# Kernel optimization log

Hardware: AMD Instinct MI355X
Metric: run time of the kernel (lower is better)

The kernel has to match this reference:

```python
import jax, jax.numpy as jnp
import numpy as np

EMBED = 1024
HEADS = 16
HEAD_DIM = EMBED // HEADS


def setup_inputs() -> dict:
    key = jax.random.key(0)
    ks = jax.random.split(key, 9)
    s = 1.0 / np.sqrt(EMBED)
    x = jax.random.normal(ks[0], (2, 2048, EMBED), dtype=jnp.float32)
    Wq = jax.random.uniform(ks[1], (EMBED, EMBED), jnp.float32, -s, s)
    bq = jax.random.uniform(ks[2], (EMBED,), jnp.float32, -s, s)
    Wk = jax.random.uniform(ks[3], (EMBED, EMBED), jnp.float32, -s, s)
    bk = jax.random.uniform(ks[4], (EMBED,), jnp.float32, -s, s)
    Wv = jax.random.uniform(ks[5], (EMBED, EMBED), jnp.float32, -s, s)
    bv = jax.random.uniform(ks[6], (EMBED,), jnp.float32, -s, s)
    Wo = jax.random.uniform(ks[7], (EMBED, EMBED), jnp.float32, -s, s)
    bo = jax.random.uniform(ks[8], (EMBED,), jnp.float32, -s, s)
    return {"x": x, "Wq": Wq, "bq": bq, "Wk": Wk, "bk": bk,
            "Wv": Wv, "bv": bv, "Wo": Wo, "bo": bo}


def reference(x, Wq, bq, Wk, bk, Wv, bv, Wo, bo):
    B, S, E = x.shape
    H, D = HEADS, HEAD_DIM
    # QKV projections, split heads: [B,S,E] -> [B,H,S,D]
    def proj(W, b):
        return (x @ W + b).reshape(B, S, H, D).transpose(0, 2, 1, 3)
    q, k, v = proj(Wq, bq), proj(Wk, bk), proj(Wv, bv)
    scores = jnp.einsum('bhsd,bhtd->bhst', q, k) / jnp.sqrt(jnp.float32(D))
    attn = jax.nn.softmax(scores, axis=-1)
    out = jnp.einsum('bhst,bhtd->bhsd', attn, v)  # [B,H,S,D]
    out = out.transpose(0, 2, 1, 3).reshape(B, S, E)
    return out @ Wo + bo
```

## Files before the change

kernel.cpp:

```cpp
#include <hip/hip_runtime.h>
#include <cstddef>
#include <cstdint>

#define EMB 1024
#define NH 16
#define HD 64
#define SEQ 2048
#define BATCH 2
#define MROWS 4096
#define LOG2E 1.4426950408889634f

typedef unsigned short u16;
typedef __attribute__((ext_vector_type(8))) short short8;
typedef __attribute__((ext_vector_type(4))) short short4v;
typedef __attribute__((ext_vector_type(4))) float floatx4;

#define MFMA32(a,b,c) __builtin_amdgcn_mfma_f32_16x16x32_bf16((a),(b),(c),0,0,0)

#if __has_builtin(__builtin_amdgcn_mfma_f32_16x16x16bf16_1k)
#define PVMFMA(a,b,c) __builtin_amdgcn_mfma_f32_16x16x16bf16_1k((a),(b),(c),0,0,0)
#elif __has_builtin(__builtin_amdgcn_mfma_f32_16x16x16_bf16)
#define PVMFMA(a,b,c) __builtin_amdgcn_mfma_f32_16x16x16_bf16((a),(b),(c),0,0,0)
#else
__device__ __forceinline__ floatx4 pv_mfma_fb(short4v a, short4v b, floatx4 c) {
    short8 a8 = {a.x, a.y, a.z, a.w, 0, 0, 0, 0};
    short8 b8 = {b.x, b.y, b.z, b.w, 0, 0, 0, 0};
    return MFMA32(a8, b8, c);
}
#define PVMFMA(a,b,c) pv_mfma_fb((a),(b),(c))
#endif

__device__ __forceinline__ u16 f2bf(float f) {
    union { float f; uint32_t u; } v; v.f = f;
    return (u16)((v.u + 0x7fffu + ((v.u >> 16) & 1u)) >> 16);
}
__device__ __forceinline__ uint32_t pk_trunc(float a, float b) {
    union { float f; uint32_t u; } va, vb; va.f = a; vb.f = b;
    return __builtin_amdgcn_perm(vb.u, va.u, 0x07060302u);
}
__device__ __forceinline__ float lo_f(uint32_t u) {
    union { uint32_t u; float f; } v; v.u = u << 16; return v.f;
}
__device__ __forceinline__ float hi_f(uint32_t u) {
    union { uint32_t u; float f; } v; v.u = u & 0xffff0000u; return v.f;
}
typedef const __attribute__((address_space(1))) void* gptr_t;
typedef __attribute__((address_space(3))) void* lptr_t;
__device__ __forceinline__ void gl2lds16(const void* g, void* l) {
    __builtin_amdgcn_global_load_lds((gptr_t)g, (lptr_t)l, 16, 0, 0);
}

__global__ __launch_bounds__(256) void cvt_all_k(
    const float* __restrict__ x,
    const float* __restrict__ W0, const float* __restrict__ W1,
    const float* __restrict__ W2, const float* __restrict__ W3,
    u16* __restrict__ Wt4, u16* __restrict__ xh) {
    const int z = blockIdx.z;
    const int tid = threadIdx.x;
    if (z == 4) {
        const int nb = gridDim.x * gridDim.y;
        const int bid = blockIdx.y * gridDim.x + blockIdx.x;
        const int stride = nb * 256 * 8;
        for (int i = (bid * 256 + tid) * 8; i < MROWS * EMB; i += stride) {
            float4 a = *(const float4*)(x + i);
            float4 b = *(const float4*)(x + i + 4);
            alignas(16) u16 o[8] = {f2bf(a.x), f2bf(a.y), f2bf(a.z), f2bf(a.w),
                                    f2bf(b.x), f2bf(b.y), f2bf(b.z), f2bf(b.w)};
            *(uint4*)(xh + i) = *(const uint4*)o;
        }
        return;
    }
    const float* W = (z == 0) ? W0 : (z == 1) ? W1 : (z == 2) ? W2 : W3;
    const float scale = (z == 0) ? 0.125f * LOG2E : 1.0f;
    u16* dst = Wt4 + (size_t)z * 1048576;
    __shared__ float Lf[64][65];
    const int kt = blockIdx.y * 64, nt = blockIdx.x * 64;
    {
        const int r = tid >> 2, c4 = (tid & 3) * 16;
        const float* src = W + (size_t)(kt + r) * EMB + nt + c4;
        #pragma unroll
        for (int i = 0; i < 16; i += 4) {
            float4 v = *(const float4*)(src + i);
            Lf[r][c4 + i + 0] = v.x; Lf[r][c4 + i + 1] = v.y;
            Lf[r][c4 + i + 2] = v.z; Lf[r][c4 + i + 3] = v.w;
        }
    }
    __syncthreads();
    const int n = tid >> 2, k4 = (tid & 3) * 16;
    alignas(16) u16 hb[16];
    #pragma unroll
    for (int i = 0; i < 16; ++i) hb[i] = f2bf(Lf[k4 + i][n] * scale);
    const size_t o = (size_t)(nt + n) * EMB + kt + k4;
    *(uint4*)(dst + o) = *(const uint4*)hb;
    *(uint4*)(dst + o + 8) = *(const uint4*)(hb + 8);
}

__global__ __launch_bounds__(256) void gemm_qkv_k(
    const u16* __restrict__ xh, const u16* __restrict__ Wt4,
    const float* __restrict__ b0, const float* __restrict__ b1,
    const float* __restrict__ b2,
    u16* __restrict__ Q, u16* __restrict__ K, u16* __restrict__ Vt) {
    const int z = blockIdx.z;
    const u16* Wt = Wt4 + (size_t)z * 1048576;
    const float* bias = (z == 0) ? b0 : (z == 1) ? b1 : b2;
    const float bscale = (z == 0) ? 0.125f * LOG2E : 1.0f;
    const int bm = blockIdx.y * 128, bn = blockIdx.x * 128;
    __shared__ alignas(16) u16 As[4096];
    __shared__ alignas(16) u16 Bs[4096];
    const int tid = threadIdx.x;
    const int lane = tid & 63, w = tid >> 6;
    const int l15 = lane & 15, quad = lane >> 4;
    const int wm = (w & 1) * 64, wn = (w >> 1) * 64;

    floatx4 acc[4][4];
    const floatx4 zf = {0.f, 0.f, 0.f, 0.f};
    #pragma unroll
    for (int mt = 0; mt < 4; ++mt)
        #pragma unroll
        for (int nt = 0; nt < 4; ++nt) acc[mt][nt] = zf;

    const int c0 = tid, c1 = tid + 256;
    const int r0 = c0 >> 2, p0 = c0 & 3, cc0 = (p0 - r0 - (r0 >> 2)) & 3;
    const int r1 = c1 >> 2, p1 = c1 & 3, cc1 = (p1 - r1 - (r1 >> 2)) & 3;
    const u16* ag0 = xh + (size_t)(bm + r0) * EMB + cc0 * 8;
    const u16* ag1 = xh + (size_t)(bm + r1) * EMB + cc1 * 8;
    const u16* bg0 = Wt + (size_t)(bn + r0) * EMB + cc0 * 8;
    const u16* bg1 = Wt + (size_t)(bn + r1) * EMB + cc1 * 8;

    for (int kt = 0; kt < EMB; kt += 32) {
        __syncthreads();
        gl2lds16(ag0 + kt, &As[c0 * 8]); gl2lds16(ag1 + kt, &As[c1 * 8]);
        gl2lds16(bg0 + kt, &Bs[c0 * 8]); gl2lds16(bg1 + kt, &Bs[c1 * 8]);
        __syncthreads();
        short8 af[4], bf[4];
        #pragma unroll
        for (int t = 0; t < 4; ++t) {
            const int ra = wm + t * 16 + l15;
            const int rb = wn + t * 16 + l15;
            af[t] = *(const short8*)&As[ra * 32 + ((quad + ra + (ra >> 2)) & 3) * 8];
            bf[t] = *(const short8*)&Bs[rb * 32 + ((quad + rb + (rb >> 2)) & 3) * 8];
        }
        #pragma unroll
        for (int mt = 0; mt < 4; ++mt)
            #pragma unroll
            for (int nt = 0; nt < 4; ++nt)
                acc[mt][nt] = MFMA32(af[mt], bf[nt], acc[mt][nt]);
    }

    if (z != 2) {
        u16* out = (z == 0) ? Q : K;
        #pragma unroll
        for (int nt = 0; nt < 4; ++nt) {
            const int col = bn + wn + nt * 16 + l15;
            const float bv = bias[col] * bscale;
            #pragma unroll
            for (int mt = 0; mt < 4; ++mt) {
                const int row = bm + wm + mt * 16 + quad * 4;
                #pragma unroll
                for (int r = 0; r < 4; ++r)
                    out[(size_t)(row + r) * EMB + col] = f2bf(acc[mt][nt][r] + bv);
            }
        }
    } else {
        #pragma unroll
        for (int nt = 0; nt < 4; ++nt) {
            const int col = bn + wn + nt * 16 + l15;
            const int hh = col >> 6, d = col & 63;
            const float bv = bias[col];
            #pragma unroll
            for (int mt = 0; mt < 4; ++mt) {
                const int row = bm + wm + mt * 16 + quad * 4;
                const int bb = row >> 11, t0 = row & 2047;
                alignas(8) u16 pk4[4];
                #pragma unroll
                for (int r = 0; r < 4; ++r) pk4[r] = f2bf(acc[mt][nt][r] + bv);
                *(uint2*)(Vt + ((size_t)((bb * NH + hh) * HD + d)) * SEQ + t0) =
                    *(const uint2*)pk4;
            }
        }
    }
}

__global__ __launch_bounds__(256) void gemm_o_k(
    const u16* __restrict__ Ag, const u16* __restrict__ Wt,
    const float* __restrict__ bias, float* __restrict__ out) {
    const int bm = blockIdx.y * 128, bn = blockIdx.x * 64;
    __shared__ alignas(16) u16 As[4096];
    __shared__ alignas(16) u16 Bs[2048];
    const int tid = threadIdx.x;
    const int lane = tid & 63, w = tid >> 6;
    const int l15 = lane & 15, quad = lane >> 4;
    const int wm = w * 32;

    floatx4 acc[2][4];
    const floatx4 zf = {0.f, 0.f, 0.f, 0.f};
    #pragma unroll
    for (int mt = 0; mt < 2; ++mt)
        #pragma unroll
        for (int nt = 0; nt < 4; ++nt) acc[mt][nt] = zf;

    const int c0 = tid, c1 = tid + 256;
    const int r0 = c0 >> 2, p0 = c0 & 3, cc0 = (p0 - r0 - (r0 >> 2)) & 3;
    const int r1 = c1 >> 2, p1 = c1 & 3, cc1 = (p1 - r1 - (r1 >> 2)) & 3;
    const u16* ag0 = Ag + (size_t)(bm + r0) * EMB + cc0 * 8;
    const u16* ag1 = Ag + (size_t)(bm + r1) * EMB + cc1 * 8;
    const u16* bg0 = Wt + (size_t)(bn + r0) * EMB + cc0 * 8;

    for (int kt = 0; kt < EMB; kt += 32) {
        __syncthreads();
        gl2lds16(ag0 + kt, &As[c0 * 8]);
        gl2lds16(ag1 + kt, &As[c1 * 8]);
        if (c0 < 256) gl2lds16(bg0 + kt, &Bs[c0 * 8]);
        __syncthreads();
        short8 af[2], bf[4];
        #pragma unroll
        for (int t = 0; t < 2; ++t) {
            const int ra = wm + t * 16 + l15;
            af[t] = *(const short8*)&As[ra * 32 + ((quad + ra + (ra >> 2)) & 3) * 8];
        }
        #pragma unroll
        for (int t = 0; t < 4; ++t) {
            const int rb = t * 16 + l15;
            bf[t] = *(const short8*)&Bs[rb * 32 + ((quad + rb + (rb >> 2)) & 3) * 8];
        }
        #pragma unroll
        for (int mt = 0; mt < 2; ++mt)
            #pragma unroll
            for (int nt = 0; nt < 4; ++nt)
                acc[mt][nt] = MFMA32(af[mt], bf[nt], acc[mt][nt]);
    }

    #pragma unroll
    for (int nt = 0; nt < 4; ++nt) {
        const int col = bn + nt * 16 + l15;
        const float bv = bias[col];
        #pragma unroll
        for (int mt = 0; mt < 2; ++mt) {
            const int row = bm + wm + mt * 16 + quad * 4;
            #pragma unroll
            for (int r = 0; r < 4; ++r)
                out[(size_t)(row + r) * EMB + col] = acc[mt][nt][r] + bv;
        }
    }
}

__global__ __launch_bounds__(256) void flash_k(
    const u16* __restrict__ Q, const u16* __restrict__ K,
    const u16* __restrict__ Vt,
    u16* __restrict__ Np0, u16* __restrict__ Np1,
    u16* __restrict__ Np2, u16* __restrict__ Np3,
    float* __restrict__ Lp) {
    const int qt = blockIdx.x, h = blockIdx.y;
    const int b = blockIdx.z >> 2, sp = blockIdx.z & 3;
    const int t0 = sp * (SEQ / 4);
    __shared__ alignas(16) u16 Ks[4096];
    __shared__ alignas(16) u16 Vs[4096];
    const int tid = threadIdx.x;
    const int lane = tid & 63, w = tid >> 6;
    const int l15 = lane & 15, quad = lane >> 4;

    const u16* qp = Q + (size_t)(b * SEQ + qt * 128 + w * 32 + l15) * EMB + h * HD + quad * 8;
    short8 qb[2][2];
    qb[0][0] = *(const short8*)qp;
    qb[0][1] = *(const short8*)(qp + 32);
    qb[1][0] = *(const short8*)(qp + 16 * EMB);
    qb[1][1] = *(const short8*)(qp + 16 * EMB + 32);

    const floatx4 zf = {0.f, 0.f, 0.f, 0.f};
    floatx4 oacc[2][4];
    float l_part[2] = {0.f, 0.f};
    #pragma unroll
    for (int u = 0; u < 2; ++u)
        #pragma unroll
        for (int nt = 0; nt < 4; ++nt) oacc[u][nt] = zf;

    const int s0 = tid, s1 = tid + 256;
    const int kr0 = s0 >> 3, kc0 = ((s0 & 7) - kr0) & 7;
    const int kr1 = s1 >> 3, kc1 = ((s1 & 7) - kr1) & 7;
    const u16* kg0 = K + (size_t)(b * SEQ + t0 + kr0) * EMB + h * HD + kc0 * 8;
    const u16* kg1 = K + (size_t)(b * SEQ + t0 + kr1) * EMB + h * HD + kc1 * 8;
    const u16* vg0 = Vt + ((size_t)((b * NH + h) * HD + kr0)) * SEQ + t0 + kc0 * 8;
    const u16* vg1 = Vt + ((size_t)((b * NH + h) * HD + kr1)) * SEQ + t0 + kc1 * 8;

    for (int kt = 0; kt < SEQ / 4 / 64; ++kt) {
        __syncthreads();
        gl2lds16(kg0 + (size_t)kt * 64 * EMB, &Ks[s0 * 8]);
        gl2lds16(kg1 + (size_t)kt * 64 * EMB, &Ks[s1 * 8]);
        gl2lds16(vg0 + kt * 64, &Vs[s0 * 8]);
        gl2lds16(vg1 + kt * 64, &Vs[s1 * 8]);
        __syncthreads();

        floatx4 sa[2][4];
        #pragma unroll
        for (int mt = 0; mt < 4; ++mt) {
            const int r = mt * 16 + l15;
            const short8 ka0 = *(const short8*)&Ks[r * 64 + ((quad + r) & 7) * 8];
            const short8 ka1 = *(const short8*)&Ks[r * 64 + ((quad + 4 + r) & 7) * 8];
            #pragma unroll
            for (int u = 0; u < 2; ++u)
                sa[u][mt] = MFMA32(ka1, qb[u][1], MFMA32(ka0, qb[u][0], zf));
        }

        short4v pfr[2][4];
        #pragma unroll
        for (int u = 0; u < 2; ++u)
            #pragma unroll
            for (int mt = 0; mt < 4; ++mt) {
                const float e0 = exp2f(sa[u][mt][0]);
                const float e1 = exp2f(sa[u][mt][1]);
                const float e2 = exp2f(sa[u][mt][2]);
                const float e3 = exp2f(sa[u][mt][3]);
                const uint32_t u01 = pk_trunc(e0, e1);
                const uint32_t u23 = pk_trunc(e2, e3);
                l_part[u] += (lo_f(u01) + hi_f(u01)) + (lo_f(u23) + hi_f(u23));
                union { uint32_t uu[2]; short4v s; } pk;
                pk.uu[0] = u01; pk.uu[1] = u23;
                pfr[u][mt] = pk.s;
            }

        #pragma unroll
        for (int mt = 0; mt < 4; ++mt) {
            const int c16 = mt * 2 + (quad >> 1);
            const int hof = (quad & 1) * 4;
            #pragma unroll
            for (int nt = 0; nt < 4; ++nt) {
                const int vr = nt * 16 + l15;
                const short4v vb =
                    *(const short4v*)&Vs[vr * 64 + ((c16 + vr) & 7) * 8 + hof];
                #pragma unroll
                for (int u = 0; u < 2; ++u)
                    oacc[u][nt] = PVMFMA(pfr[u][mt], vb, oacc[u][nt]);
            }
        }
    }

    u16* np = (sp == 0) ? Np0 : (sp == 1) ? Np1 : (sp == 2) ? Np2 : Np3;
    float* lp = Lp + (size_t)sp * (MROWS * NH);

    #pragma unroll
    for (int u = 0; u < 2; ++u) {
        l_part[u] += __shfl_xor(l_part[u], 16, 64);
        l_part[u] += __shfl_xor(l_part[u], 32, 64);
        if (quad == 0) {
            const int qrow = qt * 128 + w * 32 + u * 16 + l15;
            lp[(size_t)(b * SEQ + qrow) * NH + h] = l_part[u];
        }
    }

    #pragma unroll
    for (int u = 0; u < 2; ++u)
        #pragma unroll
        for (int r = 0; r < 4; ++r) {
            const size_t o =
                (size_t)(b * SEQ + qt * 128 + w * 32 + u * 16 + quad * 4 + r) * EMB
                + h * HD + l15;
            #pragma unroll
            for (int nt = 0; nt < 4; ++nt)
                np[o + nt * 16] = f2bf(oacc[u][nt][r]);
        }
}

__global__ __launch_bounds__(256) void reduce_k(
    const u16* __restrict__ Np0, const u16* __restrict__ Np1,
    const u16* __restrict__ Np2, const u16* __restrict__ Np3,
    const float* __restrict__ Lp, u16* __restrict__ AO) {
    const int i = blockIdx.x * 256 + threadIdx.x;
    const int e = i * 4;
    const int row = e >> 10;
    const int hh = (e & 1023) >> 6;
    const size_t lx = (size_t)row * NH + hh;
    const float lsum = Lp[lx] + Lp[(size_t)(MROWS * NH) + lx] +
                       Lp[2 * (size_t)(MROWS * NH) + lx] +
                       Lp[3 * (size_t)(MROWS * NH) + lx];
    const float inv = 1.f / lsum;
    const uint2 n0 = *(const uint2*)(Np0 + e);
    const uint2 n1 = *(const uint2*)(Np1 + e);
    const uint2 n2 = *(const uint2*)(Np2 + e);
    const uint2 n3 = *(const uint2*)(Np3 + e);
    const float x0 = (lo_f(n0.x) + lo_f(n1.x) + lo_f(n2.x) + lo_f(n3.x)) * inv;
    const float x1 = (hi_f(n0.x) + hi_f(n1.x) + hi_f(n2.x) + hi_f(n3.x)) * inv;
    const float x2 = (lo_f(n0.y) + lo_f(n1.y) + lo_f(n2.y) + lo_f(n3.y)) * inv;
    const float x3 = (hi_f(n0.y) + hi_f(n1.y) + hi_f(n2.y) + hi_f(n3.y)) * inv;
    uint2 o;
    o.x = (uint32_t)f2bf(x0) | ((uint32_t)f2bf(x1) << 16);
    o.y = (uint32_t)f2bf(x2) | ((uint32_t)f2bf(x3) << 16);
    *(uint2*)(AO + e) = o;
}

extern "C" void kernel_launch(void* const* d_in, const int* in_sizes, int n_in,
                              void* d_out, int out_size, void* d_ws, size_t ws_size,
                              hipStream_t stream) {
    const float* x  = (const float*)d_in[0];
    const float* Wq = (const float*)d_in[1];
    const float* bq = (const float*)d_in[2];
    const float* Wk = (const float*)d_in[3];
    const float* bk = (const float*)d_in[4];
    const float* Wv = (const float*)d_in[5];
    const float* bv = (const float*)d_in[6];
    const float* Wo = (const float*)d_in[7];
    const float* bo = (const float*)d_in[8];

    u16* ws16 = (u16*)d_ws;
    const size_t P4 = (size_t)MROWS * EMB;
    u16* xh  = ws16;
    u16* Qb  = ws16 + P4;
    u16* Kb  = ws16 + 2 * P4;
    u16* Vtb = ws16 + 3 * P4;
    u16* Wt4 = ws16 + 4 * P4;
    u16* N1  = ws16 + 5 * P4;
    u16* N2  = ws16 + 6 * P4;
    u16* N3  = ws16 + 7 * P4;
    float* Lp = (float*)(ws16 + 8 * P4);

    cvt_all_k<<<dim3(16, 16, 5), 256, 0, stream>>>(x, Wq, Wk, Wv, Wo, Wt4, xh);
    gemm_qkv_k<<<dim3(8, 32, 3), 256, 0, stream>>>(xh, Wt4, bq, bk, bv, Qb, Kb, Vtb);
    flash_k<<<dim3(16, 16, 8), 256, 0, stream>>>(Qb, Kb, Vtb, xh, N1, N2, N3, Lp);
    reduce_k<<<4096, 256, 0, stream>>>(xh, N1, N2, N3, Lp, Qb);
    gemm_o_k<<<dim3(16, 32, 1), 256, 0, stream>>>(Qb, Wt4 + 3 * 1048576, bo, (float*)d_out);
}
```

Before: 235.4 us.

## Use bit-trick exp2, MFMA row sums, and separate V transpose kernel

Softmax exp2 is replaced by a Schraudolph-style bit trick: fmaf(s, 2^23, 1064992512) cast to int gives approximate float bits, which are packed straight to bf16. The row-sum reduction moves from scalar adds plus shuffles to an extra MFMA against a vector of ones. The strided transposed V store in the QKV GEMM epilogue is replaced by a plain row-major store followed by a new LDS-based transpose kernel. The aim is to cut transcendental and VALU work in the attention inner loop and to make the GEMM V writes coalesced, at the cost of an extra launch, extra traffic through the V buffer, and a coarse exp approximation that may hurt accuracy.

```diff
diff --git a/kernel.cpp b/kernel.cpp
--- a/kernel.cpp
+++ b/kernel.cpp
@@ -34,15 +34,17 @@
     union { float f; uint32_t u; } v; v.f = f;
     return (u16)((v.u + 0x7fffu + ((v.u >> 16) & 1u)) >> 16);
 }
-__device__ __forceinline__ uint32_t pk_trunc(float a, float b) {
-    union { float f; uint32_t u; } va, vb; va.f = a; vb.f = b;
-    return __builtin_amdgcn_perm(vb.u, va.u, 0x07060302u);
+__device__ __forceinline__ uint32_t pk2u(uint32_t a, uint32_t b) {
+    return __builtin_amdgcn_perm(b, a, 0x07060302u);
 }
 __device__ __forceinline__ float lo_f(uint32_t u) {
     union { uint32_t u; float f; } v; v.u = u << 16; return v.f;
 }
 __device__ __forceinline__ float hi_f(uint32_t u) {
     union { uint32_t u; float f; } v; v.u = u & 0xffff0000u; return v.f;
+}
+__device__ __forceinline__ uint32_t exp2_fast_bits(float s) {
+    return (uint32_t)(int)fmaf(s, 8388608.0f, 1064992512.0f);
 }
 typedef const __attribute__((address_space(1))) void* gptr_t;
 typedef __attribute__((address_space(3))) void* lptr_t;
@@ -99,10 +101,11 @@
     const u16* __restrict__ xh, const u16* __restrict__ Wt4,
     const float* __restrict__ b0, const float* __restrict__ b1,
     const float* __restrict__ b2,
-    u16* __restrict__ Q, u16* __restrict__ K, u16* __restrict__ Vt) {
+    u16* __restrict__ Q, u16* __restrict__ K, u16* __restrict__ V) {
     const int z = blockIdx.z;
     const u16* Wt = Wt4 + (size_t)z * 1048576;
     const float* bias = (z == 0) ? b0 : (z == 1) ? b1 : b2;
+    u16* out = (z == 0) ? Q : (z == 1) ? K : V;
     const float bscale = (z == 0) ? 0.125f * LOG2E : 1.0f;
     const int bm = blockIdx.y * 128, bn = blockIdx.x * 128;
     __shared__ alignas(16) u16 As[4096];
@@ -147,36 +150,16 @@
                 acc[mt][nt] = MFMA32(af[mt], bf[nt], acc[mt][nt]);
     }
 
-    if (z != 2) {
-        u16* out = (z == 0) ? Q : K;
-        #pragma unroll
-        for (int nt = 0; nt < 4; ++nt) {
-            const int col = bn + wn + nt * 16 + l15;
-            const float bv = bias[col] * bscale;
-            #pragma unroll
-            for (int mt = 0; mt < 4; ++mt) {
-                const int row = bm + wm + mt * 16 + quad * 4;
-                #pragma unroll
-                for (int r = 0; r < 4; ++r)
-                    out[(size_t)(row + r) * EMB + col] = f2bf(acc[mt][nt][r] + bv);
-            }
-        }
-    } else {
-        #pragma unroll
-        for (int nt = 0; nt < 4; ++nt) {
-            const int col = bn + wn + nt * 16 + l15;
-            const int hh = col >> 6, d = col & 63;
-            const float bv = bias[col];
-            #pragma unroll
-            for (int mt = 0; mt < 4; ++mt) {
-                const int row = bm + wm + mt * 16 + quad * 4;
-                const int bb = row >> 11, t0 = row & 2047;
-                alignas(8) u16 pk4[4];
-                #pragma unroll
-                for (int r = 0; r < 4; ++r) pk4[r] = f2bf(acc[mt][nt][r] + bv);
-                *(uint2*)(Vt + ((size_t)((bb * NH + hh) * HD + d)) * SEQ + t0) =
-                    *(const uint2*)pk4;
-            }
+    #pragma unroll
+    for (int nt = 0; nt < 4; ++nt) {
+        const int col = bn + wn + nt * 16 + l15;
+        const float bv = bias[col] * bscale;
+        #pragma unroll
+        for (int mt = 0; mt < 4; ++mt) {
+            const int row = bm + wm + mt * 16 + quad * 4;
+            #pragma unroll
+            for (int r = 0; r < 4; ++r)
+                out[(size_t)(row + r) * EMB + col] = f2bf(acc[mt][nt][r] + bv);
         }
     }
 }
@@ -242,6 +225,27 @@
                 out[(size_t)(row + r) * EMB + col] = acc[mt][nt][r] + bv;
         }
     }
+}
+
+__global__ __launch_bounds__(256) void vtrans_k(const u16* __restrict__ V,
+                                                u16* __restrict__ Vt) {
+    const int tt = blockIdx.x, h = blockIdx.y, b = blockIdx.z;
+    __shared__ u16 Lt[64][72];
+    const int tid = threadIdx.x;
+    {
+        const int r = tid >> 2, c4 = (tid & 3) * 16;
+        const u16* src = V + (size_t)(b * SEQ + tt * 64 + r) * EMB + h * HD + c4;
+        alignas(16) u16 buf[16];
+        *(uint4*)buf = *(const uint4*)src;
+        *(uint4*)(buf + 8) = *(const uint4*)(src + 8);
+        #pragma unroll
+        for (int i = 0; i < 16; ++i) Lt[c4 + i][r] = buf[i];
+    }
+    __syncthreads();
+    const int d = tid >> 2, t4 = (tid & 3) * 16;
+    u16* dst = Vt + ((size_t)((b * NH + h) * HD + d)) * SEQ + tt * 64 + t4;
+    *(uint4*)dst = *(const uint4*)&Lt[d][t4];
+    *(uint4*)(dst + 8) = *(const uint4*)&Lt[d][t4 + 8];
 }
 
 __global__ __launch_bounds__(256) void flash_k(
@@ -267,12 +271,15 @@
     qb[1][1] = *(const short8*)(qp + 16 * EMB + 32);
 
     const floatx4 zf = {0.f, 0.f, 0.f, 0.f};
+    const short4v vones = {0x3F80, 0x3F80, 0x3F80, 0x3F80};
     floatx4 oacc[2][4];
-    float l_part[2] = {0.f, 0.f};
-    #pragma unroll
-    for (int u = 0; u < 2; ++u)
+    floatx4 lacc[2];
+    #pragma unroll
+    for (int u = 0; u < 2; ++u) {
+        lacc[u] = zf;
         #pragma unroll
         for (int nt = 0; nt < 4; ++nt) oacc[u][nt] = zf;
+    }
 
     const int s0 = tid, s1 = tid + 256;
     const int kr0 = s0 >> 3, kc0 = ((s0 & 7) - kr0) & 7;
@@ -306,15 +313,13 @@
         for (int u = 0; u < 2; ++u)
             #pragma unroll
             for (int mt = 0; mt < 4; ++mt) {
-                const float e0 = exp2f(sa[u][mt][0]);
-                const float e1 = exp2f(sa[u][mt][1]);
-                const float e2 = exp2f(sa[u][mt][2]);
-                const float e3 = exp2f(sa[u][mt][3]);
-                const uint32_t u01 = pk_trunc(e0, e1);
-                const uint32_t u23 = pk_trunc(e2, e3);
-                l_part[u] += (lo_f(u01) + hi_f(u01)) + (lo_f(u23) + hi_f(u23));
+                const uint32_t e0 = exp2_fast_bits(sa[u][mt][0]);
+                const uint32_t e1 = exp2_fast_bits(sa[u][mt][1]);
+                const uint32_t e2 = exp2_fast_bits(sa[u][mt][2]);
+                const uint32_t e3 = exp2_fast_bits(sa[u][mt][3]);
                 union { uint32_t uu[2]; short4v s; } pk;
-                pk.uu[0] = u01; pk.uu[1] = u23;
+                pk.uu[0] = pk2u(e0, e1);
+                pk.uu[1] = pk2u(e2, e3);
                 pfr[u][mt] = pk.s;
             }
 
@@ -331,6 +336,9 @@
                 for (int u = 0; u < 2; ++u)
                     oacc[u][nt] = PVMFMA(pfr[u][mt], vb, oacc[u][nt]);
             }
+            #pragma unroll
+            for (int u = 0; u < 2; ++u)
+                lacc[u] = PVMFMA(pfr[u][mt], vones, lacc[u]);
         }
     }
 
@@ -338,14 +346,14 @@
     float* lp = Lp + (size_t)sp * (MROWS * NH);
 
     #pragma unroll
-    for (int u = 0; u < 2; ++u) {
-        l_part[u] += __shfl_xor(l_part[u], 16, 64);
-        l_part[u] += __shfl_xor(l_part[u], 32, 64);
-        if (quad == 0) {
-            const int qrow = qt * 128 + w * 32 + u * 16 + l15;
-            lp[(size_t)(b * SEQ + qrow) * NH + h] = l_part[u];
-        }
-    }
+    for (int u = 0; u < 2; ++u)
+        if (l15 == 0) {
+            #pragma unroll
+            for (int r = 0; r < 4; ++r) {
+                const int qrow = qt * 128 + w * 32 + u * 16 + quad * 4 + r;
+                lp[(size_t)(b * SEQ + qrow) * NH + h] = lacc[u][r];
+            }
+        }
 
     #pragma unroll
     for (int u = 0; u < 2; ++u)
@@ -405,16 +413,17 @@
     u16* xh  = ws16;
     u16* Qb  = ws16 + P4;
     u16* Kb  = ws16 + 2 * P4;
-    u16* Vtb = ws16 + 3 * P4;
-    u16* Wt4 = ws16 + 4 * P4;
-    u16* N1  = ws16 + 5 * P4;
+    u16* Vb  = ws16 + 3 * P4;
+    u16* Vtb = ws16 + 4 * P4;
+    u16* Wt4 = ws16 + 5 * P4;
     u16* N2  = ws16 + 6 * P4;
     u16* N3  = ws16 + 7 * P4;
     float* Lp = (float*)(ws16 + 8 * P4);
 
     cvt_all_k<<<dim3(16, 16, 5), 256, 0, stream>>>(x, Wq, Wk, Wv, Wo, Wt4, xh);
-    gemm_qkv_k<<<dim3(8, 32, 3), 256, 0, stream>>>(xh, Wt4, bq, bk, bv, Qb, Kb, Vtb);
-    flash_k<<<dim3(16, 16, 8), 256, 0, stream>>>(Qb, Kb, Vtb, xh, N1, N2, N3, Lp);
-    reduce_k<<<4096, 256, 0, stream>>>(xh, N1, N2, N3, Lp, Qb);
+    gemm_qkv_k<<<dim3(8, 32, 3), 256, 0, stream>>>(xh, Wt4, bq, bk, bv, Qb, Kb, Vb);
+    vtrans_k<<<dim3(32, 16, 2), 256, 0, stream>>>(Vb, Vtb);
+    flash_k<<<dim3(16, 16, 8), 256, 0, stream>>>(Qb, Kb, Vtb, xh, Vb, N2, N3, Lp);
+    reduce_k<<<4096, 256, 0, stream>>>(xh, Vb, N2, N3, Lp, Qb);
     gemm_o_k<<<dim3(16, 32, 1), 256, 0, stream>>>(Qb, Wt4 + 3 * 1048576, bo, (float*)d_out);
 }
```

After: 207.1 us. -12.0%, faster.
